# Kernel optimization log

Measured on AMD Instinct MI355X. Metric: run time of the kernel, lower is better.

## Reference

```python
import jax, jax.numpy as jnp
import numpy as np
from jax import lax

B, C_IN, C_OUT, H, W = 2, 128, 256, 128, 128
KH = KW = 3
K = KH * KW  # 9 kernel sampling locations
EPS = 1e-5


def setup_inputs() -> dict:
    ks = jax.random.split(jax.random.key(0), 9)
    x = jax.random.normal(ks[0], (B, C_IN, H, W), dtype=jnp.float32)
    # offset/mask conv: 27 = 3*K output channels, 3x3 kernel, stride 1, same pad
    w_off = jax.random.normal(ks[1], (3 * K, C_IN, KH, KW), dtype=jnp.float32) * 0.01
    b_off = jnp.zeros((3 * K,), dtype=jnp.float32)
    # deformable conv weight [C_out, C_in, 3, 3] + bias
    w_dcn = jax.random.normal(ks[2], (C_OUT, C_IN, KH, KW), dtype=jnp.float32) * (1.0 / np.sqrt(C_IN * K))
    b_dcn = jax.random.normal(ks[3], (C_OUT,), dtype=jnp.float32) * 0.01
    # BatchNorm (inference-mode) params
    gamma = 1.0 + 0.1 * jax.random.normal(ks[4], (C_OUT,), dtype=jnp.float32)
    beta = 0.1 * jax.random.normal(ks[5], (C_OUT,), dtype=jnp.float32)
    moving_mean = 0.1 * jax.random.normal(ks[6], (C_OUT,), dtype=jnp.float32)
    moving_var = jax.random.uniform(ks[7], (C_OUT,), dtype=jnp.float32, minval=0.5, maxval=1.5)
    return {"x": x, "w_off": w_off, "b_off": b_off, "w_dcn": w_dcn, "b_dcn": b_dcn,
            "gamma": gamma, "beta": beta, "moving_mean": moving_mean, "moving_var": moving_var}


def _conv2d_nchw(x, w, b):
    y = lax.conv_general_dilated(x, w, window_strides=(1, 1), padding='SAME',
                                 dimension_numbers=('NCHW', 'OIHW', 'NCHW'))
    return y + b[None, :, None, None]


def _bilinear_gather(x, yi, xi):
    """Gather x[b,:,yi,xi] with zero padding outside. x:[B,C,H,W]; yi,xi:[B,K,H,W] int."""
    valid = ((yi >= 0) & (yi < H) & (xi >= 0) & (xi < W)).astype(x.dtype)  # [B,K,H,W]
    yc = jnp.clip(yi, 0, H - 1)
    xc = jnp.clip(xi, 0, W - 1)
    idx = (yc * W + xc).reshape(B, -1)  # [B, K*H*W]
    xf = x.reshape(B, C_IN, H * W)
    g = jax.vmap(lambda xb, ib: xb[:, ib])(xf, idx)  # [B, C, K*H*W]
    return g.reshape(B, C_IN, K, H, W) * valid[:, None]


def _deform_conv(x, offset, mask, w, b):
    """DCNv2 modulated deformable conv, 3x3, stride 1, SAME (pad=1).
    offset: [B, 2K, H, W] with (dy, dx) interleaved per kernel location (tfa/DCNv2 layout).
    mask:   [B, K, H, W] (already sigmoided).
    """
    dy = offset[:, 0::2]  # [B,K,H,W]
    dx = offset[:, 1::2]
    ky = (jnp.arange(K, dtype=jnp.float32) // KW) - 1.0  # kernel y offsets in {-1,0,1}
    kx = (jnp.arange(K, dtype=jnp.float32) % KW) - 1.0
    ii = jnp.arange(H, dtype=jnp.float32)[:, None]
    jj = jnp.arange(W, dtype=jnp.float32)[None, :]
    py = ii[None, None] + ky[None, :, None, None] + dy  # [B,K,H,W] sampling y
    px = jj[None, None] + kx[None, :, None, None] + dx  # [B,K,H,W] sampling x

    y0f = jnp.floor(py)
    x0f = jnp.floor(px)
    wy = (py - y0f)[:, None]  # [B,1,K,H,W]
    wx = (px - x0f)[:, None]
    y0 = y0f.astype(jnp.int32)
    x0 = x0f.astype(jnp.int32)

    v00 = _bilinear_gather(x, y0, x0)
    v01 = _bilinear_gather(x, y0, x0 + 1)
    v10 = _bilinear_gather(x, y0 + 1, x0)
    v11 = _bilinear_gather(x, y0 + 1, x0 + 1)
    val = (v00 * (1 - wy) * (1 - wx) + v01 * (1 - wy) * wx
           + v10 * wy * (1 - wx) + v11 * wy * wx)  # [B,C,K,H,W]
    val = val * mask[:, None]  # modulation

    w_r = w.reshape(C_OUT, C_IN, K)
    out = jnp.einsum('bckhw,ock->bohw', val, w_r)
    return out + b[None, :, None, None]


def reference(x, w_off, b_off, w_dcn, b_dcn, gamma, beta, moving_mean, moving_var):
    weight_info = _conv2d_nchw(x, w_off, b_off)  # [B, 27, H, W]
    o1, o2, m = jnp.split(weight_info, 3, axis=1)
    offset = jnp.concatenate((o1, o2), axis=1)  # [B, 18, H, W]
    mask = jax.nn.sigmoid(m)  # [B, 9, H, W]
    y = _deform_conv(x, offset, mask, w_dcn, b_dcn)
    # BatchNorm2d (inference, channels_first) + ReLU
    inv = gamma / jnp.sqrt(moving_var + EPS)
    y = (y - moving_mean[None, :, None, None]) * inv[None, :, None, None] + beta[None, :, None, None]
    return jax.nn.relu(y)
```

## Files before the change

### kernel.cpp

```cpp
#include <hip/hip_runtime.h>
#include <hip/hip_fp16.h>

#define HH 128
#define WW 128
#define CIN 128
#define COUT 256
#define K9 9
#define HW (HH*WW)
#define PIX (2*HW)
#define KDIM (CIN*K9)
#define BN_EPS 1e-5f

typedef __attribute__((ext_vector_type(8))) short short8;
typedef __attribute__((ext_vector_type(4))) float f32x4;
typedef _Float16 half8 __attribute__((ext_vector_type(8)));
typedef unsigned short u16;
typedef unsigned int u32;

union H8 { short8 s; __half2 h2[4]; half8 h; };

struct __align__(16) Meta16 { ushort4 idx; __half2 w01, w23; };
static_assert(sizeof(Meta16) == 16, "");

__device__ __forceinline__ u16 f2h(float f) {
    union { __half h; u16 u; } x; x.h = __float2half_rn(f); return x.u;
}

__global__ __launch_bounds__(256) void prep_xt(const float* __restrict__ x,
                                               u16* __restrict__ xt) {
    __shared__ float tile[32][129];
    const int b   = blockIdx.y;
    const int hw0 = blockIdx.x * 32;
    const float* __restrict__ xb = x + (size_t)b * (CIN*HW);
    #pragma unroll
    for (int i = 0; i < 16; ++i) {
        const int idx = threadIdx.x + i*256;
        const int c = idx >> 5, hwl = idx & 31;
        tile[hwl][c] = xb[(size_t)c*HW + hw0 + hwl];
    }
    __syncthreads();
    const int hwl = threadIdx.x >> 3;
    const int c0  = (threadIdx.x & 7) * 16;
    short8 s0, s1;
    #pragma unroll
    for (int j = 0; j < 8; ++j) {
        s0[j] = (short)f2h(tile[hwl][c0 + j]);
        s1[j] = (short)f2h(tile[hwl][c0 + 8 + j]);
    }
    u16* dst = xt + ((size_t)b*HW + hw0 + hwl)*CIN + c0;
    *(short8*)dst = s0;
    *(short8*)(dst + 8) = s1;
}

__global__ __launch_bounds__(128) void prep_wall(const float* __restrict__ w_dcn,
                                                 const float* __restrict__ w_off,
                                                 u16* __restrict__ wT2,
                                                 u16* __restrict__ wOffT2) {
    const int c = threadIdx.x;
    const int k = blockIdx.x;
    const int o = blockIdx.y;
    const int s = c >> 5, ch = c & 31;
    const int tt = k*4 + s;
    if (o < COUT) {
        wT2[((size_t)tt*COUT + o)*32 + ch] = f2h(w_dcn[(size_t)o*KDIM + c*K9 + k]);
    } else {
        const int j = o - COUT;
        wOffT2[((size_t)tt*32 + j)*32 + ch] =
            (j < 27) ? f2h(w_off[(size_t)j*KDIM + c*K9 + k]) : (u16)0;
    }
}

__global__ __launch_bounds__(1024, 4) __attribute__((amdgpu_waves_per_eu(4, 4)))
void dcn_fused(
    const u16* __restrict__ xt, const u16* __restrict__ wT2,
    const u16* __restrict__ wOffT2, const float* __restrict__ b_off,
    const float* __restrict__ b_dcn, const float* __restrict__ gamma,
    const float* __restrict__ beta, const float* __restrict__ mmean,
    const float* __restrict__ mvar, float* __restrict__ out)
{
    __shared__ __align__(16) u16 Vs[128*128];
    __shared__ __align__(16) Meta16 metaL[K9*128];
    float* wiL = (float*)&Vs[0];

    const int t = threadIdx.x, l = t & 63, wv = t >> 6;
    const int l15 = l & 15, lq = l >> 4;
    const int bid = (blockIdx.x & 7) * 32 + (blockIdx.x >> 3);
    const int pg0 = bid * 128;
    const int b   = pg0 >> 14;
    const int hw0 = pg0 & 16383;
    const u16* __restrict__ xtb = xt + (size_t)b * (HW*CIN);

    {
        const int pxg = wv >> 1;
        const int jh  = wv & 1;
        const int px  = pxg*16 + l15;
        const int pg  = pg0 + px;
        const int hw  = pg & 16383;
        const int h = hw >> 7, w = hw & 127;
        f32x4 oa = {0.f,0.f,0.f,0.f};
        #pragma unroll
        for (int tt = 0; tt < 36; ++tt) {
            const int k = tt >> 2, c0 = (tt & 3) * 32;
            const int yy = h + (k/3) - 1, xx = w + (k%3) - 1;
            const bool valid = ((unsigned)yy < HH) && ((unsigned)xx < WW);
            const int idx = min(max(yy,0),HH-1)*WW + min(max(xx,0),WW-1);
            H8 bv, av;
            bv.s = *(const short8*)(xtb + (size_t)idx*CIN + c0 + lq*8);
            av.s = *(const short8*)(wOffT2 + ((size_t)tt*32 + jh*16 + l15)*32 + lq*8);
            if (!valid) bv.s = (short8){0,0,0,0,0,0,0,0};
            oa = __builtin_amdgcn_mfma_f32_16x16x32_f16(av.h, bv.h, oa, 0,0,0);
        }
        #pragma unroll
        for (int r = 0; r < 4; ++r)
            wiL[px*33 + jh*16 + lq*4 + r] = oa[r];
        __syncthreads();

        #pragma unroll
        for (int rd = 0; rd < 2; ++rd) {
            const int u = t + rd*1024;
            if (u < 1152) {
                const int px2 = u & 127, k = u >> 7;
                const int hwp = (pg0 + px2) & 16383;
                const int hp = hwp >> 7, wp = hwp & 127;
                const float dy = wiL[px2*33 + 2*k]     + b_off[2*k];
                const float dx = wiL[px2*33 + 2*k + 1] + b_off[2*k+1];
                const float mm = wiL[px2*33 + 18 + k]  + b_off[18+k];
                const float py = (float)hp + (float)(k/3) - 1.0f + dy;
                const float px_ = (float)wp + (float)(k%3) - 1.0f + dx;
                const float msk = 1.0f / (1.0f + expf(-mm));
                const float y0f = floorf(py), x0f = floorf(px_);
                const float wy = py - y0f, wx = px_ - x0f;
                const int y0 = (int)y0f, x0 = (int)x0f;
                const int y1 = y0 + 1,   x1 = x0 + 1;
                const bool v00 = ((unsigned)y0 < HH) && ((unsigned)x0 < WW);
                const bool v01 = ((unsigned)y0 < HH) && ((unsigned)x1 < WW);
                const bool v10 = ((unsigned)y1 < HH) && ((unsigned)x0 < WW);
                const bool v11 = ((unsigned)y1 < HH) && ((unsigned)x1 < WW);
                const int y0c = min(max(y0,0),HH-1), y1c = min(max(y1,0),HH-1);
                const int x0c = min(max(x0,0),WW-1), x1c = min(max(x1,0),WW-1);
                Meta16 mo;
                mo.idx.x = (u16)(y0c*WW + x0c);
                mo.idx.y = (u16)(y0c*WW + x1c);
                mo.idx.z = (u16)(y1c*WW + x0c);
                mo.idx.w = (u16)(y1c*WW + x1c);
                const float f00 = v00 ? (1.f-wy)*(1.f-wx)*msk : 0.f;
                const float f01 = v01 ? (1.f-wy)*wx*msk       : 0.f;
                const float f10 = v10 ? wy*(1.f-wx)*msk       : 0.f;
                const float f11 = v11 ? wy*wx*msk             : 0.f;
                mo.w01 = __floats2half2_rn(f00, f01);
                mo.w23 = __floats2half2_rn(f10, f11);
                metaL[k*128 + px2] = mo;
            }
        }
        __syncthreads();
    }

    const int pxl  = t >> 3;
    const int cb   = t & 7;
    const int px15 = pxl & 15;

    f32x4 acc[8];
    #pragma unroll
    for (int n = 0; n < 8; ++n) acc[n] = (f32x4){0.f,0.f,0.f,0.f};

    const u16 *g0, *g1, *g2, *g3;
    __half2 wb0, wb1, wb2, wb3;

#define SETMETA(k_) do { \
    const Meta16 mt_ = metaL[(k_)*128 + pxl]; \
    g0 = xtb + (size_t)mt_.idx.x*CIN + cb*8; \
    g1 = xtb + (size_t)mt_.idx.y*CIN + cb*8; \
    g2 = xtb + (size_t)mt_.idx.z*CIN + cb*8; \
    g3 = xtb + (size_t)mt_.idx.w*CIN + cb*8; \
    wb0 = __half2half2(__low2half(mt_.w01)); \
    wb1 = __half2half2(__high2half(mt_.w01)); \
    wb2 = __half2half2(__low2half(mt_.w23)); \
    wb3 = __half2half2(__high2half(mt_.w23)); \
} while (0)

#define ISSUE(cr_, u_) do { \
    cr_[0].s = *(const short8*)(g0 + (u_)*64); \
    cr_[1].s = *(const short8*)(g1 + (u_)*64); \
    cr_[2].s = *(const short8*)(g2 + (u_)*64); \
    cr_[3].s = *(const short8*)(g3 + (u_)*64); \
} while (0)

#define COMBINE_WRITE(cr_, u_) do { \
    H8 r_; \
    _Pragma("unroll") \
    for (int i_ = 0; i_ < 4; ++i_) \
        r_.h2[i_] = __hfma2(cr_[3].h2[i_], wb3, __hfma2(cr_[2].h2[i_], wb2, \
                    __hfma2(cr_[1].h2[i_], wb1, __hmul2(cr_[0].h2[i_], wb0)))); \
    *(short8*)&Vs[pxl*128 + ((cb + (u_)*8) ^ px15)*8] = r_.s; \
} while (0)

    H8 cA[4], cB[4];
    SETMETA(0);
    ISSUE(cA, 0); ISSUE(cB, 1);
    COMBINE_WRITE(cA, 0); COMBINE_WRITE(cB, 1);
    __syncthreads();

    for (int k = 0; k < 9; ++k) {
        const bool pf = (k < 8);
        H8 av[4];
        #pragma unroll
        for (int s = 0; s < 4; ++s)
            av[s].s = *(const short8*)
                (wT2 + ((size_t)(k*4 + s)*COUT + wv*16 + l15)*32 + lq*8);
        __builtin_amdgcn_sched_barrier(0);
        if (pf) { SETMETA(k+1); ISSUE(cA, 0); ISSUE(cB, 1); }
        __builtin_amdgcn_sched_barrier(0);

        #pragma unroll
        for (int s = 0; s < 4; ++s) {
            #pragma unroll
            for (int nh = 0; nh < 2; ++nh) {
                H8 bf[4];
                #pragma unroll
                for (int j = 0; j < 4; ++j) {
                    const int n = nh*4 + j;
                    bf[j].s = *(const short8*)
                        &Vs[(n*16 + l15)*128 + ((s*4 + lq) ^ l15)*8];
                }
                #pragma unroll
                for (int j = 0; j < 4; ++j)
                    acc[nh*4 + j] = __builtin_amdgcn_mfma_f32_16x16x32_f16(
                                        av[s].h, bf[j].h, acc[nh*4 + j], 0, 0, 0);
            }
        }
        __syncthreads();
        if (pf) { COMBINE_WRITE(cA, 0); COMBINE_WRITE(cB, 1); }
        __syncthreads();
    }
#undef SETMETA
#undef ISSUE
#undef COMBINE_WRITE

    float sc[4], sh[4];
    #pragma unroll
    for (int r = 0; r < 4; ++r) {
        const int o = wv*16 + lq*4 + r;
        sc[r] = gamma[o] * rsqrtf(mvar[o] + BN_EPS);
        sh[r] = (b_dcn[o] - mmean[o]) * sc[r] + beta[o];
    }
    #pragma unroll
    for (int n = 0; n < 8; ++n) {
        #pragma unroll
        for (int r = 0; r < 4; ++r) {
            const int o = wv*16 + lq*4 + r;
            float* __restrict__ op = out + ((size_t)(b*COUT + o) << 14) + hw0;
            const float v = fmaf(acc[n][r], sc[r], sh[r]);
            op[n*16 + l15] = fmaxf(v, 0.f);
        }
    }
}

extern "C" void kernel_launch(void* const* d_in, const int* in_sizes, int n_in,
                              void* d_out, int out_size, void* d_ws, size_t ws_size,
                              hipStream_t stream) {
    (void)in_sizes; (void)n_in; (void)out_size; (void)ws_size;
    const float* x      = (const float*)d_in[0];
    const float* w_off  = (const float*)d_in[1];
    const float* b_off  = (const float*)d_in[2];
    const float* w_dcn  = (const float*)d_in[3];
    const float* b_dcn  = (const float*)d_in[4];
    const float* gamma  = (const float*)d_in[5];
    const float* beta   = (const float*)d_in[6];
    const float* mmean  = (const float*)d_in[7];
    const float* mvar   = (const float*)d_in[8];
    float* out = (float*)d_out;

    char* ws = (char*)d_ws;
    u16* xtp    = (u16*)ws;
    u16* wT2    = (u16*)(ws + 8388608);
    u16* wOffT2 = (u16*)(ws + 8388608 + 589824);

    prep_xt  <<<dim3(HW/32, 2), 256, 0, stream>>>(x, xtp);
    prep_wall<<<dim3(9, 288), 128, 0, stream>>>(w_dcn, w_off, wT2, wOffT2);
    dcn_fused<<<dim3(PIX/128), 1024, 0, stream>>>(xtp, wT2, wOffT2, b_off, b_dcn,
                                                  gamma, beta, mmean, mvar, out);
}
```

Baseline: 72.84 us.

## Halve pixel tile per block, double-buffer LDS gather, and widen per-wave output tile

```diff
diff --git a/kernel.cpp b/kernel.cpp
--- a/kernel.cpp
+++ b/kernel.cpp
@@ -70,7 +70,7 @@
     }
 }
 
-__global__ __launch_bounds__(1024, 4) __attribute__((amdgpu_waves_per_eu(4, 4)))
+__global__ __launch_bounds__(512, 4) __attribute__((amdgpu_waves_per_eu(4, 4)))
 void dcn_fused(
     const u16* __restrict__ xt, const u16* __restrict__ wT2,
     const u16* __restrict__ wOffT2, const float* __restrict__ b_off,
@@ -78,14 +78,14 @@
     const float* __restrict__ beta, const float* __restrict__ mmean,
     const float* __restrict__ mvar, float* __restrict__ out)
 {
-    __shared__ __align__(16) u16 Vs[128*128];
-    __shared__ __align__(16) Meta16 metaL[K9*128];
-    float* wiL = (float*)&Vs[0];
+    __shared__ __align__(16) u16 Vs[2][64*128];
+    __shared__ __align__(16) Meta16 metaL[K9*64];
+    float* wiL = (float*)&Vs[0][0];
 
     const int t = threadIdx.x, l = t & 63, wv = t >> 6;
     const int l15 = l & 15, lq = l >> 4;
-    const int bid = (blockIdx.x & 7) * 32 + (blockIdx.x >> 3);
-    const int pg0 = bid * 128;
+    const int bid = (blockIdx.x & 7) * 64 + (blockIdx.x >> 3);
+    const int pg0 = bid * 64;
     const int b   = pg0 >> 14;
     const int hw0 = pg0 & 16383;
     const u16* __restrict__ xtb = xt + (size_t)b * (HW*CIN);
@@ -117,9 +117,9 @@
 
         #pragma unroll
         for (int rd = 0; rd < 2; ++rd) {
-            const int u = t + rd*1024;
-            if (u < 1152) {
-                const int px2 = u & 127, k = u >> 7;
+            const int u = t + rd*512;
+            if (u < 576) {
+                const int px2 = u & 63, k = u >> 6;
                 const int hwp = (pg0 + px2) & 16383;
                 const int hp = hwp >> 7, wp = hwp & 127;
                 const float dy = wiL[px2*33 + 2*k]     + b_off[2*k];
@@ -149,7 +149,7 @@
                 const float f11 = v11 ? wy*wx*msk             : 0.f;
                 mo.w01 = __floats2half2_rn(f00, f01);
                 mo.w23 = __floats2half2_rn(f10, f11);
-                metaL[k*128 + px2] = mo;
+                metaL[k*64 + px2] = mo;
             }
         }
         __syncthreads();
@@ -161,13 +161,13 @@
 
     f32x4 acc[8];
     #pragma unroll
-    for (int n = 0; n < 8; ++n) acc[n] = (f32x4){0.f,0.f,0.f,0.f};
+    for (int i = 0; i < 8; ++i) acc[i] = (f32x4){0.f,0.f,0.f,0.f};
 
     const u16 *g0, *g1, *g2, *g3;
     __half2 wb0, wb1, wb2, wb3;
 
 #define SETMETA(k_) do { \
-    const Meta16 mt_ = metaL[(k_)*128 + pxl]; \
+    const Meta16 mt_ = metaL[(k_)*64 + pxl]; \
     g0 = xtb + (size_t)mt_.idx.x*CIN + cb*8; \
     g1 = xtb + (size_t)mt_.idx.y*CIN + cb*8; \
     g2 = xtb + (size_t)mt_.idx.z*CIN + cb*8; \
@@ -185,28 +185,31 @@
     cr_[3].s = *(const short8*)(g3 + (u_)*64); \
 } while (0)
 
-#define COMBINE_WRITE(cr_, u_) do { \
+#define COMBINE_WRITE(cr_, u_, buf_) do { \
     H8 r_; \
     _Pragma("unroll") \
     for (int i_ = 0; i_ < 4; ++i_) \
         r_.h2[i_] = __hfma2(cr_[3].h2[i_], wb3, __hfma2(cr_[2].h2[i_], wb2, \
                     __hfma2(cr_[1].h2[i_], wb1, __hmul2(cr_[0].h2[i_], wb0)))); \
-    *(short8*)&Vs[pxl*128 + ((cb + (u_)*8) ^ px15)*8] = r_.s; \
+    *(short8*)&Vs[buf_][pxl*128 + ((cb + (u_)*8) ^ px15)*8] = r_.s; \
 } while (0)
 
     H8 cA[4], cB[4];
     SETMETA(0);
     ISSUE(cA, 0); ISSUE(cB, 1);
-    COMBINE_WRITE(cA, 0); COMBINE_WRITE(cB, 1);
+    COMBINE_WRITE(cA, 0, 0); COMBINE_WRITE(cB, 1, 0);
     __syncthreads();
 
+    int cur = 0;
     for (int k = 0; k < 9; ++k) {
         const bool pf = (k < 8);
-        H8 av[4];
+        H8 av[4][2];
         #pragma unroll
         for (int s = 0; s < 4; ++s)
-            av[s].s = *(const short8*)
-                (wT2 + ((size_t)(k*4 + s)*COUT + wv*16 + l15)*32 + lq*8);
+            #pragma unroll
+            for (int m = 0; m < 2; ++m)
+                av[s][m].s = *(const short8*)
+                    (wT2 + ((size_t)(k*4 + s)*COUT + wv*32 + m*16 + l15)*32 + lq*8);
         __builtin_amdgcn_sched_barrier(0);
         if (pf) { SETMETA(k+1); ISSUE(cA, 0); ISSUE(cB, 1); }
         __builtin_amdgcn_sched_barrier(0);
@@ -215,42 +218,43 @@
         for (int s = 0; s < 4; ++s) {
             #pragma unroll
             for (int nh = 0; nh < 2; ++nh) {
-                H8 bf[4];
+                H8 bf[2];
                 #pragma unroll
-                for (int j = 0; j < 4; ++j) {
-                    const int n = nh*4 + j;
+                for (int j = 0; j < 2; ++j) {
+                    const int n = nh*2 + j;
                     bf[j].s = *(const short8*)
-                        &Vs[(n*16 + l15)*128 + ((s*4 + lq) ^ l15)*8];
+                        &Vs[cur][(n*16 + l15)*128 + ((s*4 + lq) ^ l15)*8];
                 }
                 #pragma unroll
-                for (int j = 0; j < 4; ++j)
-                    acc[nh*4 + j] = __builtin_amdgcn_mfma_f32_16x16x32_f16(
-                                        av[s].h, bf[j].h, acc[nh*4 + j], 0, 0, 0);
+                for (int m = 0; m < 2; ++m)
+                    #pragma unroll
+                    for (int j = 0; j < 2; ++j)
+                        acc[m*4 + nh*2 + j] =
+                            __builtin_amdgcn_mfma_f32_16x16x32_f16(
+                                av[s][m].h, bf[j].h, acc[m*4 + nh*2 + j], 0, 0, 0);
             }
         }
+        if (pf) { COMBINE_WRITE(cA, 0, cur ^ 1); COMBINE_WRITE(cB, 1, cur ^ 1); }
         __syncthreads();
-        if (pf) { COMBINE_WRITE(cA, 0); COMBINE_WRITE(cB, 1); }
-        __syncthreads();
+        cur ^= 1;
     }
 #undef SETMETA
 #undef ISSUE
 #undef COMBINE_WRITE
 
-    float sc[4], sh[4];
-    #pragma unroll
-    for (int r = 0; r < 4; ++r) {
-        const int o = wv*16 + lq*4 + r;
-        sc[r] = gamma[o] * rsqrtf(mvar[o] + BN_EPS);
-        sh[r] = (b_dcn[o] - mmean[o]) * sc[r] + beta[o];
-    }
-    #pragma unroll
-    for (int n = 0; n < 8; ++n) {
+    #pragma unroll
+    for (int m = 0; m < 2; ++m) {
         #pragma unroll
         for (int r = 0; r < 4; ++r) {
-            const int o = wv*16 + lq*4 + r;
+            const int o = wv*32 + m*16 + lq*4 + r;
+            const float sc = gamma[o] * rsqrtf(mvar[o] + BN_EPS);
+            const float sh = (b_dcn[o] - mmean[o]) * sc + beta[o];
             float* __restrict__ op = out + ((size_t)(b*COUT + o) << 14) + hw0;
-            const float v = fmaf(acc[n][r], sc[r], sh[r]);
-            op[n*16 + l15] = fmaxf(v, 0.f);
+            #pragma unroll
+            for (int n = 0; n < 4; ++n) {
+                const float v = fmaf(acc[m*4 + n][r], sc, sh);
+                op[n*16 + l15] = fmaxf(v, 0.f);
+            }
         }
     }
 }
@@ -277,6 +281,6 @@
 
     prep_xt  <<<dim3(HW/32, 2), 256, 0, stream>>>(x, xtp);
     prep_wall<<<dim3(9, 288), 128, 0, stream>>>(w_dcn, w_off, wT2, wOffT2);
-    dcn_fused<<<dim3(PIX/128), 1024, 0, stream>>>(xtp, wT2, wOffT2, b_off, b_dcn,
-                                                  gamma, beta, mmean, mvar, out);
-}
+    dcn_fused<<<dim3(PIX/64), 512, 0, stream>>>(xtp, wT2, wOffT2, b_off, b_dcn,
+                                                gamma, beta, mmean, mvar, out);
+}
```

New measurement: 73.39 us. Within noise of the previous version (+0.8%).
